# Kernel optimization log

Hardware: AMD Instinct MI355X
Metric: run time of the kernel (lower is better)

## Reference

```python
import jax, jax.numpy as jnp
import numpy as np

B, S, D_IN, D_OUT = 8, 2048, 1024, 1024


def setup_inputs() -> dict:
    key = jax.random.key(0)
    kx, kq, kk, kv = jax.random.split(key, 4)
    x = jax.random.normal(kx, (B, S, D_IN), dtype=jnp.float32)
    # torch nn.Linear weight is (d_out, d_in); we store the transpose (d_in, d_out)
    # and apply as x @ W, same math. Scale ~ kaiming-uniform-ish magnitude.
    scale = 1.0 / np.sqrt(D_IN)
    Wq = jax.random.normal(kq, (D_IN, D_OUT), dtype=jnp.float32) * scale
    Wk = jax.random.normal(kk, (D_IN, D_OUT), dtype=jnp.float32) * scale
    Wv = jax.random.normal(kv, (D_IN, D_OUT), dtype=jnp.float32) * scale
    return {"x": x, "Wq": Wq, "Wk": Wk, "Wv": Wv}


def reference(x, Wq, Wk, Wv):
    # x: (b, s, d_in) -> (b, s, d_out). Single-head causal attention, dropout=0.
    b, s, _ = x.shape
    q = jnp.einsum('bsd,de->bse', x, Wq)
    k = jnp.einsum('bsd,de->bse', x, Wk)
    v = jnp.einsum('bsd,de->bse', x, Wv)
    d_k = k.shape[-1]
    scores = jnp.einsum('bqe,bke->bqk', q, k) / jnp.sqrt(jnp.float32(d_k))
    # causal mask: position t attends to 0..t (strict upper triangle -> -inf)
    causal = jnp.tril(jnp.ones((s, s), dtype=bool))
    scores = jnp.where(causal[None, :, :], scores, -jnp.inf)
    weights = jax.nn.softmax(scores, axis=-1)
    return jnp.einsum('bqk,bke->bqe', weights, v)
```

## Files before the change

### kernel.cpp

```cpp
#include <hip/hip_runtime.h>


#define Bv 8
#define Sv 2048
#define Dv 1024
#define BK 32
#define NT 16

typedef _Float16 f16x8 __attribute__((ext_vector_type(8)));
typedef _Float16 f16x4 __attribute__((ext_vector_type(4)));
typedef float    f32x4 __attribute__((ext_vector_type(4)));

#define GLL(gp, lp)                                            \
  __builtin_amdgcn_global_load_lds(                            \
      (const __attribute__((address_space(1))) void*)(gp),     \
      (__attribute__((address_space(3))) void*)(lp), 16, 0, 0)

__device__ __forceinline__ void mma_step(const _Float16* As, const _Float16* Bs,
                                         int wm, int wn, int lane, f32x4 acc[4][4]) {
  int ll = lane & 15, quad = lane >> 4;
  f16x8 a[4], b[4];
#pragma unroll
  for (int mi = 0; mi < 4; ++mi)
    a[mi] = *(const f16x8*)(As + (wm * 64 + mi * 16 + ll) * BK + quad * 8);
#pragma unroll
  for (int ni = 0; ni < 4; ++ni)
    b[ni] = *(const f16x8*)(Bs + (wn * 64 + ni * 16 + ll) * BK + quad * 8);
#pragma unroll
  for (int mi = 0; mi < 4; ++mi)
#pragma unroll
    for (int ni = 0; ni < 4; ++ni)
      acc[mi][ni] = __builtin_amdgcn_mfma_f32_16x16x32_f16(a[mi], b[ni], acc[mi][ni], 0, 0, 0);
}

__device__ __forceinline__ void gemm_dbuf(const _Float16* __restrict__ A, int lda,
                                          const _Float16* __restrict__ B, int ldb,
                                          int ktiles, _Float16 (*S)[4096],
                                          f32x4 acc[4][4]) {
  const int tid  = threadIdx.x;
  const int lane = tid & 63, wave = tid >> 6;
  const int wm = wave >> 1, wn = wave & 1;
  const int srow = wave * 32 + (lane >> 2);
  const int scol = (lane & 3) * 8;
  const int loA0 = srow * lda + scol, loA1 = loA0 + 16 * lda;
  const int loB0 = srow * ldb + scol, loB1 = loB0 + 16 * ldb;
  _Float16* dA = &S[0][wave * 1024];
  _Float16* dB = &S[1][wave * 1024];
  const _Float16* gA = A;
  const _Float16* gB = B;

#define STAGE(bi)                              \
  do {                                         \
    GLL(gA + loA0, dA + (bi) * 8192);          \
    GLL(gA + loA1, dA + (bi) * 8192 + 512);    \
    GLL(gB + loB0, dB + (bi) * 8192);          \
    GLL(gB + loB1, dB + (bi) * 8192 + 512);    \
  } while (0)

  STAGE(0);
  for (int kt = 0; kt < ktiles; kt += 2) {
    __syncthreads();
    gA += BK; gB += BK;
    STAGE(1);
    mma_step(S[0], S[1], wm, wn, lane, acc);
    __syncthreads();
    gA += BK; gB += BK;
    if (kt + 2 < ktiles) STAGE(0);
    mma_step(S[2], S[3], wm, wn, lane, acc);
  }
#undef STAGE
}

#define ZERO_ACC(acc)                              \
  _Pragma("unroll") for (int i_ = 0; i_ < 4; ++i_) \
  _Pragma("unroll") for (int j_ = 0; j_ < 4; ++j_) \
      acc[i_][j_] = (f32x4){0.f, 0.f, 0.f, 0.f};

__global__ __launch_bounds__(256) void ca_cast(const float* __restrict__ x,
                                               _Float16* __restrict__ y) {
  int i = (blockIdx.x * 256 + threadIdx.x) * 8;
  f32x4 a = *(const f32x4*)(x + i);
  f32x4 b = *(const f32x4*)(x + i + 4);
  f16x8 h;
#pragma unroll
  for (int j = 0; j < 4; ++j) { h[j] = (_Float16)a[j]; h[4 + j] = (_Float16)b[j]; }
  *(f16x8*)(y + i) = h;
}

__global__ __launch_bounds__(256) void ca_transpose(const float* __restrict__ W0,
                                                    const float* __restrict__ W1,
                                                    const float* __restrict__ W2,
                                                    _Float16* __restrict__ T0,
                                                    _Float16* __restrict__ T1,
                                                    _Float16* __restrict__ T2) {
  const float* W = blockIdx.z == 0 ? W0 : blockIdx.z == 1 ? W1 : W2;
  _Float16* WT   = blockIdx.z == 0 ? T0 : blockIdx.z == 1 ? T1 : T2;
  __shared__ _Float16 t[32][33];
  int k0 = blockIdx.x * 32, n0 = blockIdx.y * 32;
  int r = threadIdx.x >> 5, c = threadIdx.x & 31;
#pragma unroll
  for (int i = 0; i < 4; ++i)
    t[r + i * 8][c] = (_Float16)W[(size_t)(k0 + r + i * 8) * Dv + n0 + c];
  __syncthreads();
#pragma unroll
  for (int i = 0; i < 4; ++i)
    WT[(size_t)(n0 + r + i * 8) * Dv + k0 + c] = t[c][r + i * 8];
}

__global__ __launch_bounds__(512, 2) void ca_qkv3(const _Float16* __restrict__ X,
                                                  const _Float16* __restrict__ WTq,
                                                  const _Float16* __restrict__ WTk,
                                                  const _Float16* __restrict__ WTv,
                                                  _Float16* __restrict__ Q,
                                                  _Float16* __restrict__ K,
                                                  _Float16* __restrict__ Vt) {
  __shared__ _Float16 L[8][8192];

  int id  = blockIdx.x;
  int swz = (id & 7) * 96 + (id >> 3);
  int my  = swz / 12, nt = swz - my * 12;
  int m0  = my * 256;
  int which = nt >> 2;
  int n0  = (nt & 3) * 256;
  const _Float16* WT = which == 0 ? WTq : which == 1 ? WTk : WTv;
  const _Float16* gA = X + (size_t)m0 * Dv;
  const _Float16* gB = WT + (size_t)n0 * Dv;

  const int tid  = threadIdx.x;
  const int lane = tid & 63, wave = tid >> 6;
  const int wm = wave >> 2, wn = wave & 3;
  const int ll = lane & 15, quad = lane >> 4;

  const int laneRow = wave * 8 + (lane >> 3);
  const int laneCol = (((lane & 7) ^ ((lane >> 3) & 7)) << 3);
  const int gOff0 = laneRow * Dv + laneCol;
  const int gOff1 = (64 + laneRow) * Dv + laneCol;
  _Float16* Ldst = &L[0][0] + wave * 512;

  const int sw0 = ((quad ^ (ll & 7)) << 3);
  _Float16* Lb = &L[0][0];
  const _Float16* pA0 = Lb + wm * 8192 + ll * 64 + sw0;
  const _Float16* pA1 = Lb + wm * 8192 + ll * 64 + (sw0 ^ 32);
  const _Float16* pB0 = Lb + 16384 + (wn >> 1) * 8192 + (wn & 1) * 4096 + ll * 64 + sw0;
  const _Float16* pB1 = Lb + 16384 + (wn >> 1) * 8192 + (wn & 1) * 4096 + ll * 64 + (sw0 ^ 32);

#define STG(slot, mat, ht, kpf)                                   \
  do {                                                            \
    const _Float16* g_ = (mat) + (size_t)((ht) * 128 * Dv + (kpf) * 64); \
    GLL(g_ + gOff0, Ldst + (slot) * 8192);                        \
    GLL(g_ + gOff1, Ldst + (slot) * 8192 + 4096);                 \
  } while (0)

#define RD_A(P, d, mh)                                            \
  _Pragma("unroll") for (int i_ = 0; i_ < 4; ++i_)                \
      a[i_] = *(const f16x8*)((P) + (d) * 32768 + ((mh) * 4 + i_) * 1024);
#define RD_B(P, d)                                                \
  _Pragma("unroll") for (int i_ = 0; i_ < 4; ++i_)                \
      b[i_] = *(const f16x8*)((P) + (d) * 32768 + i_ * 1024);
#define MMA(mh)                                                   \
  __builtin_amdgcn_s_setprio(1);                                  \
  _Pragma("unroll") for (int i_ = 0; i_ < 4; ++i_)                \
  _Pragma("unroll") for (int j_ = 0; j_ < 4; ++j_)                \
      acc[(mh) * 4 + i_][j_] = __builtin_amdgcn_mfma_f32_16x16x32_f16( \
          a[i_], b[j_], acc[(mh) * 4 + i_], 0, 0, 0)[0] == 0.f    \
          ? __builtin_amdgcn_mfma_f32_16x16x32_f16(a[i_], b[j_], acc[(mh) * 4 + i_][j_], 0, 0, 0) \
          : __builtin_amdgcn_mfma_f32_16x16x32_f16(a[i_], b[j_], acc[(mh) * 4 + i_][j_], 0, 0, 0); \
  __builtin_amdgcn_s_setprio(0);
#undef MMA
#define MMA(mh)                                                   \
  __builtin_amdgcn_s_setprio(1);                                  \
  _Pragma("unroll") for (int i_ = 0; i_ < 4; ++i_)                \
  _Pragma("unroll") for (int j_ = 0; j_ < 4; ++j_)                \
      acc[(mh) * 4 + i_][j_] = __builtin_amdgcn_mfma_f32_16x16x32_f16( \
          a[i_], b[j_], acc[(mh) * 4 + i_][j_], 0, 0, 0);         \
  __builtin_amdgcn_s_setprio(0);
#define BAR() __builtin_amdgcn_s_barrier()
#define WAITV_(n) asm volatile("s_waitcnt vmcnt(" #n ")" ::: "memory")
#define WAITV(n) WAITV_(n)
#define PH_OPEN()                                                 \
  BAR();                                                          \
  asm volatile("s_waitcnt lgkmcnt(0)" ::: "memory");              \
  __builtin_amdgcn_sched_barrier(0)

#define TILEG(kk, d, G)                                           \
  do {                                                            \
    f16x8 a[4], b[4];                                             \
    RD_A(pA0, d, 0); RD_B(pB0, d);                                \
    if ((kk) + 1 < NT) STG(4 * (1 - (d)) + 0, gA, 0, (kk) + 1);   \
    PH_OPEN(); MMA(0); BAR();                                     \
    RD_A(pA0, d, 1);                                              \
    if ((kk) + 1 < NT) STG(4 * (1 - (d)) + 1, gA, 1, (kk) + 1);   \
    PH_OPEN(); MMA(1); BAR();                                     \
    RD_A(pA1, d, 0); RD_B(pB1, d);                                \
    if ((kk) + 1 < NT) STG(4 * (1 - (d)) + 3, gB, 1, (kk) + 1);   \
    PH_OPEN(); MMA(0); BAR();                                     \
    __builtin_amdgcn_sched_barrier(0);                            \
    RD_A(pA1, d, 1);                                              \
    if ((kk) + 2 < NT) STG(4 * (d) + 2, gB, 0, (kk) + 2);         \
    PH_OPEN(); MMA(1);                                            \
    WAITV(G); BAR();                                              \
    __builtin_amdgcn_sched_barrier(0);                            \
  } while (0)

  f32x4 acc[8][4];
#pragma unroll
  for (int i = 0; i < 8; ++i)
#pragma unroll
    for (int j = 0; j < 4; ++j) acc[i][j] = (f32x4){0.f, 0.f, 0.f, 0.f};

  STG(2, gB, 0, 0);
  STG(0, gA, 0, 0);
  STG(1, gA, 1, 0);
  STG(3, gB, 1, 0);
  STG(6, gB, 0, 1);
  WAITV(2); BAR();
  __builtin_amdgcn_sched_barrier(0);

#pragma unroll 1
  for (int kk = 0; kk < NT - 2; kk += 2) {
    TILEG(kk, 0, 2);
    TILEG(kk + 1, 1, 2);
  }
  TILEG(14, 0, 0);
  TILEG(15, 1, 2);

#undef TILEG
#undef PH_OPEN
#undef MMA
#undef RD_A
#undef RD_B
#undef STG

  if (which < 2) {
    _Float16* Out = which == 0 ? Q : K;
#pragma unroll
    for (int mi = 0; mi < 8; ++mi)
#pragma unroll
      for (int ni = 0; ni < 4; ++ni) {
        int gc = n0 + wn * 64 + ni * 16 + ll;
#pragma unroll
        for (int r = 0; r < 4; ++r) {
          int gr = m0 + wm * 128 + mi * 16 + quad * 4 + r;
          Out[(size_t)gr * Dv + gc] = (_Float16)acc[mi][ni][r];
        }
      }
  } else {
#pragma unroll
    for (int mi = 0; mi < 8; ++mi)
#pragma unroll
      for (int ni = 0; ni < 4; ++ni) {
        int gc = n0 + wn * 64 + ni * 16 + ll;
        int gr = m0 + wm * 128 + mi * 16 + quad * 4;
        f16x4 v;
#pragma unroll
        for (int r = 0; r < 4; ++r) v[r] = (_Float16)acc[mi][ni][r];
        *(f16x4*)(Vt + (size_t)gc * (Bv * Sv) + gr) = v;
      }
  }
}

__global__ __launch_bounds__(256) void ca_score(const _Float16* __restrict__ Q,
                                                const _Float16* __restrict__ Km,
                                                _Float16* __restrict__ U) {
  int kt = blockIdx.x, qt = blockIdx.y, b = blockIdx.z;
  if (kt > qt) return;
  __shared__ _Float16 S[4][4096];
  f32x4 acc[4][4];
  ZERO_ACC(acc);
  const _Float16* Qb = Q + ((size_t)b * Sv + qt * 128) * Dv;
  const _Float16* Kb = Km + ((size_t)b * Sv + kt * 128) * Dv;
  gemm_dbuf(Qb, Dv, Kb, Dv, Dv / BK, S, acc);
  int lane = threadIdx.x & 63, wave = threadIdx.x >> 6;
  int wm = wave >> 1, wn = wave & 1, ll = lane & 15, quad = lane >> 4;
#pragma unroll
  for (int mi = 0; mi < 4; ++mi)
#pragma unroll
    for (int ni = 0; ni < 4; ++ni) {
      int kc = kt * 128 + wn * 64 + ni * 16 + ll;
#pragma unroll
      for (int r = 0; r < 4; ++r) {
        int qr = qt * 128 + wm * 64 + mi * 16 + quad * 4 + r;
        float s = acc[mi][ni][r] * 0.03125f;
        float u = (kc > qr) ? 0.f : __expf(fminf(fmaxf(s, -15.f), 10.f));
        U[((size_t)b * Sv + qr) * Sv + kc] = (_Float16)u;
      }
    }
}

__global__ __launch_bounds__(256) void ca_rowsum(const _Float16* __restrict__ U,
                                                 float* __restrict__ invl) {
  int rg = blockIdx.x;
  int b = rg >> 11, q = rg & (Sv - 1);
  int lim = ((q >> 7) + 1) << 7;
  const _Float16* row = U + ((size_t)b * Sv + q) * Sv;
  float s = 0.f;
  for (int k = threadIdx.x * 8; k < lim; k += 2048) {
    f16x8 v = *(const f16x8*)(row + k);
#pragma unroll
    for (int j = 0; j < 8; ++j) s += (float)v[j];
  }
#pragma unroll
  for (int o = 32; o >= 1; o >>= 1) s += __shfl_down(s, o);
  __shared__ float wsum[4];
  if ((threadIdx.x & 63) == 0) wsum[threadIdx.x >> 6] = s;
  __syncthreads();
  if (threadIdx.x == 0) invl[rg] = 1.f / (wsum[0] + wsum[1] + wsum[2] + wsum[3]);
}

__global__ __launch_bounds__(256) void ca_pv(const _Float16* __restrict__ U,
                                             const _Float16* __restrict__ Vt,
                                             const float* __restrict__ invl,
                                             float* __restrict__ Out) {
  int nt = blockIdx.x, qt = blockIdx.y, b = blockIdx.z;
  __shared__ _Float16 S[4][4096];
  f32x4 acc[4][4];
  ZERO_ACC(acc);
  const _Float16* Ab = U + ((size_t)b * Sv + qt * 128) * Sv;
  const _Float16* Bb = Vt + (size_t)(nt * 128) * (Bv * Sv) + (size_t)b * Sv;
  gemm_dbuf(Ab, Sv, Bb, Bv * Sv, (qt + 1) * 4, S, acc);
  int lane = threadIdx.x & 63, wave = threadIdx.x >> 6;
  int wm = wave >> 1, wn = wave & 1, ll = lane & 15, quad = lane >> 4;
#pragma unroll
  for (int mi = 0; mi < 4; ++mi)
#pragma unroll
    for (int ni = 0; ni < 4; ++ni) {
      int oc = nt * 128 + wn * 64 + ni * 16 + ll;
#pragma unroll
      for (int r = 0; r < 4; ++r) {
        int qr = qt * 128 + wm * 64 + mi * 16 + quad * 4 + r;
        Out[((size_t)b * Sv + qr) * Dv + oc] = acc[mi][ni][r] * invl[b * Sv + qr];
      }
    }
}

extern "C" void kernel_launch(void* const* d_in, const int* in_sizes, int n_in,
                              void* d_out, int out_size, void* d_ws, size_t ws_size,
                              hipStream_t stream) {
  const float* x  = (const float*)d_in[0];
  const float* Wq = (const float*)d_in[1];
  const float* Wk = (const float*)d_in[2];
  const float* Wv = (const float*)d_in[3];
  float* out = (float*)d_out;

  char* ws = (char*)d_ws;
  size_t off = 0;
  const size_t M = (size_t)Bv * Sv;
  _Float16* xh  = (_Float16*)(ws + off); off += M * Dv * 2;
  _Float16* WTq = (_Float16*)(ws + off); off += (size_t)Dv * Dv * 2;
  _Float16* WTk = (_Float16*)(ws + off); off += (size_t)Dv * Dv * 2;
  _Float16* WTv = (_Float16*)(ws + off); off += (size_t)Dv * Dv * 2;
  _Float16* Q   = (_Float16*)(ws + off); off += M * Dv * 2;
  _Float16* Km  = (_Float16*)(ws + off); off += M * Dv * 2;
  _Float16* Vt  = (_Float16*)(ws + off); off += M * Dv * 2;
  _Float16* U   = (_Float16*)(ws + off); off += (size_t)Bv * Sv * Sv * 2;
  float*    invl = (float*)(ws + off);   off += M * 4;

  ca_cast<<<(M * Dv) / (8 * 256), 256, 0, stream>>>(x, xh);
  ca_transpose<<<dim3(32, 32, 3), 256, 0, stream>>>(Wq, Wk, Wv, WTq, WTk, WTv);

  ca_qkv3<<<dim3(768), 512, 0, stream>>>(xh, WTq, WTk, WTv, Q, Km, Vt);

  ca_score<<<dim3(Sv / 128, Sv / 128, Bv), 256, 0, stream>>>(Q, Km, U);
  ca_rowsum<<<M, 256, 0, stream>>>(U, invl);
  ca_pv<<<dim3(Dv / 128, Sv / 128, Bv), 256, 0, stream>>>(U, Vt, invl, out);
}
```

Measured before the change: 405.2 us.

## Reuse the tuned 256x256 GEMM mainloop for the score and PV kernels

The pipelined, swizzled 256x256 mainloop from the QKV projection kernel becomes a generic gemm_fine function with configurable leading dimensions and K-tile count. The score and PV kernels now use it with 512-thread blocks, replacing the simpler 128x128 double-buffered GEMM. The goal is more data reuse per block and a better MFMA/LDS pipeline for the two attention GEMMs. The cost is coarser causal tiles, which waste more work on the diagonal, and far fewer blocks (288 score and 256 PV) with unequal work per block, which can leave CUs idle.

```diff
diff --git a/kernel.cpp b/kernel.cpp
--- a/kernel.cpp
+++ b/kernel.cpp
@@ -4,8 +4,7 @@
 #define Bv 8
 #define Sv 2048
 #define Dv 1024
-#define BK 32
-#define NT 16
+#define NTQ 16
 
 typedef _Float16 f16x8 __attribute__((ext_vector_type(8)));
 typedef _Float16 f16x4 __attribute__((ext_vector_type(4)));
@@ -15,66 +14,6 @@
   __builtin_amdgcn_global_load_lds(                            \
       (const __attribute__((address_space(1))) void*)(gp),     \
       (__attribute__((address_space(3))) void*)(lp), 16, 0, 0)
-
-__device__ __forceinline__ void mma_step(const _Float16* As, const _Float16* Bs,
-                                         int wm, int wn, int lane, f32x4 acc[4][4]) {
-  int ll = lane & 15, quad = lane >> 4;
-  f16x8 a[4], b[4];
-#pragma unroll
-  for (int mi = 0; mi < 4; ++mi)
-    a[mi] = *(const f16x8*)(As + (wm * 64 + mi * 16 + ll) * BK + quad * 8);
-#pragma unroll
-  for (int ni = 0; ni < 4; ++ni)
-    b[ni] = *(const f16x8*)(Bs + (wn * 64 + ni * 16 + ll) * BK + quad * 8);
-#pragma unroll
-  for (int mi = 0; mi < 4; ++mi)
-#pragma unroll
-    for (int ni = 0; ni < 4; ++ni)
-      acc[mi][ni] = __builtin_amdgcn_mfma_f32_16x16x32_f16(a[mi], b[ni], acc[mi][ni], 0, 0, 0);
-}
-
-__device__ __forceinline__ void gemm_dbuf(const _Float16* __restrict__ A, int lda,
-                                          const _Float16* __restrict__ B, int ldb,
-                                          int ktiles, _Float16 (*S)[4096],
-                                          f32x4 acc[4][4]) {
-  const int tid  = threadIdx.x;
-  const int lane = tid & 63, wave = tid >> 6;
-  const int wm = wave >> 1, wn = wave & 1;
-  const int srow = wave * 32 + (lane >> 2);
-  const int scol = (lane & 3) * 8;
-  const int loA0 = srow * lda + scol, loA1 = loA0 + 16 * lda;
-  const int loB0 = srow * ldb + scol, loB1 = loB0 + 16 * ldb;
-  _Float16* dA = &S[0][wave * 1024];
-  _Float16* dB = &S[1][wave * 1024];
-  const _Float16* gA = A;
-  const _Float16* gB = B;
-
-#define STAGE(bi)                              \
-  do {                                         \
-    GLL(gA + loA0, dA + (bi) * 8192);          \
-    GLL(gA + loA1, dA + (bi) * 8192 + 512);    \
-    GLL(gB + loB0, dB + (bi) * 8192);          \
-    GLL(gB + loB1, dB + (bi) * 8192 + 512);    \
-  } while (0)
-
-  STAGE(0);
-  for (int kt = 0; kt < ktiles; kt += 2) {
-    __syncthreads();
-    gA += BK; gB += BK;
-    STAGE(1);
-    mma_step(S[0], S[1], wm, wn, lane, acc);
-    __syncthreads();
-    gA += BK; gB += BK;
-    if (kt + 2 < ktiles) STAGE(0);
-    mma_step(S[2], S[3], wm, wn, lane, acc);
-  }
-#undef STAGE
-}
-
-#define ZERO_ACC(acc)                              \
-  _Pragma("unroll") for (int i_ = 0; i_ < 4; ++i_) \
-  _Pragma("unroll") for (int j_ = 0; j_ < 4; ++j_) \
-      acc[i_][j_] = (f32x4){0.f, 0.f, 0.f, 0.f};
 
 __global__ __launch_bounds__(256) void ca_cast(const float* __restrict__ x,
                                                _Float16* __restrict__ y) {
@@ -107,25 +46,10 @@
     WT[(size_t)(n0 + r + i * 8) * Dv + k0 + c] = t[c][r + i * 8];
 }
 
-__global__ __launch_bounds__(512, 2) void ca_qkv3(const _Float16* __restrict__ X,
-                                                  const _Float16* __restrict__ WTq,
-                                                  const _Float16* __restrict__ WTk,
-                                                  const _Float16* __restrict__ WTv,
-                                                  _Float16* __restrict__ Q,
-                                                  _Float16* __restrict__ K,
-                                                  _Float16* __restrict__ Vt) {
-  __shared__ _Float16 L[8][8192];
-
-  int id  = blockIdx.x;
-  int swz = (id & 7) * 96 + (id >> 3);
-  int my  = swz / 12, nt = swz - my * 12;
-  int m0  = my * 256;
-  int which = nt >> 2;
-  int n0  = (nt & 3) * 256;
-  const _Float16* WT = which == 0 ? WTq : which == 1 ? WTk : WTv;
-  const _Float16* gA = X + (size_t)m0 * Dv;
-  const _Float16* gB = WT + (size_t)n0 * Dv;
-
+__device__ __forceinline__ void gemm_fine(const _Float16* __restrict__ gA, int ldA,
+                                          const _Float16* __restrict__ gB, long ldB,
+                                          int NTt, _Float16 (*L)[8192],
+                                          f32x4 acc[8][4]) {
   const int tid  = threadIdx.x;
   const int lane = tid & 63, wave = tid >> 6;
   const int wm = wave >> 2, wn = wave & 3;
@@ -133,8 +57,10 @@
 
   const int laneRow = wave * 8 + (lane >> 3);
   const int laneCol = (((lane & 7) ^ ((lane >> 3) & 7)) << 3);
-  const int gOff0 = laneRow * Dv + laneCol;
-  const int gOff1 = (64 + laneRow) * Dv + laneCol;
+  const long aOff0 = (long)laneRow * ldA + laneCol;
+  const long aOff1 = (long)(64 + laneRow) * ldA + laneCol;
+  const long bOff0 = (long)laneRow * ldB + laneCol;
+  const long bOff1 = (long)(64 + laneRow) * ldB + laneCol;
   _Float16* Ldst = &L[0][0] + wave * 512;
 
   const int sw0 = ((quad ^ (ll & 7)) << 3);
@@ -144,29 +70,24 @@
   const _Float16* pB0 = Lb + 16384 + (wn >> 1) * 8192 + (wn & 1) * 4096 + ll * 64 + sw0;
   const _Float16* pB1 = Lb + 16384 + (wn >> 1) * 8192 + (wn & 1) * 4096 + ll * 64 + (sw0 ^ 32);
 
-#define STG(slot, mat, ht, kpf)                                   \
+#define STGA(slot, ht, kpf)                                       \
   do {                                                            \
-    const _Float16* g_ = (mat) + (size_t)((ht) * 128 * Dv + (kpf) * 64); \
-    GLL(g_ + gOff0, Ldst + (slot) * 8192);                        \
-    GLL(g_ + gOff1, Ldst + (slot) * 8192 + 4096);                 \
+    const _Float16* g_ = gA + (long)(ht) * 128 * ldA + (long)(kpf) * 64; \
+    GLL(g_ + aOff0, Ldst + (slot) * 8192);                        \
+    GLL(g_ + aOff1, Ldst + (slot) * 8192 + 4096);                 \
   } while (0)
-
+#define STGB(slot, ht, kpf)                                       \
+  do {                                                            \
+    const _Float16* g_ = gB + (long)(ht) * 128 * ldB + (long)(kpf) * 64; \
+    GLL(g_ + bOff0, Ldst + (slot) * 8192);                        \
+    GLL(g_ + bOff1, Ldst + (slot) * 8192 + 4096);                 \
+  } while (0)
 #define RD_A(P, d, mh)                                            \
   _Pragma("unroll") for (int i_ = 0; i_ < 4; ++i_)                \
       a[i_] = *(const f16x8*)((P) + (d) * 32768 + ((mh) * 4 + i_) * 1024);
 #define RD_B(P, d)                                                \
   _Pragma("unroll") for (int i_ = 0; i_ < 4; ++i_)                \
       b[i_] = *(const f16x8*)((P) + (d) * 32768 + i_ * 1024);
-#define MMA(mh)                                                   \
-  __builtin_amdgcn_s_setprio(1);                                  \
-  _Pragma("unroll") for (int i_ = 0; i_ < 4; ++i_)                \
-  _Pragma("unroll") for (int j_ = 0; j_ < 4; ++j_)                \
-      acc[(mh) * 4 + i_][j_] = __builtin_amdgcn_mfma_f32_16x16x32_f16( \
-          a[i_], b[j_], acc[(mh) * 4 + i_], 0, 0, 0)[0] == 0.f    \
-          ? __builtin_amdgcn_mfma_f32_16x16x32_f16(a[i_], b[j_], acc[(mh) * 4 + i_][j_], 0, 0, 0) \
-          : __builtin_amdgcn_mfma_f32_16x16x32_f16(a[i_], b[j_], acc[(mh) * 4 + i_][j_], 0, 0, 0); \
-  __builtin_amdgcn_s_setprio(0);
-#undef MMA
 #define MMA(mh)                                                   \
   __builtin_amdgcn_s_setprio(1);                                  \
   _Pragma("unroll") for (int i_ = 0; i_ < 4; ++i_)                \
@@ -186,51 +107,76 @@
   do {                                                            \
     f16x8 a[4], b[4];                                             \
     RD_A(pA0, d, 0); RD_B(pB0, d);                                \
-    if ((kk) + 1 < NT) STG(4 * (1 - (d)) + 0, gA, 0, (kk) + 1);   \
+    if ((kk) + 1 < NTt) STGA(4 * (1 - (d)) + 0, 0, (kk) + 1);     \
     PH_OPEN(); MMA(0); BAR();                                     \
     RD_A(pA0, d, 1);                                              \
-    if ((kk) + 1 < NT) STG(4 * (1 - (d)) + 1, gA, 1, (kk) + 1);   \
+    if ((kk) + 1 < NTt) STGA(4 * (1 - (d)) + 1, 1, (kk) + 1);     \
     PH_OPEN(); MMA(1); BAR();                                     \
     RD_A(pA1, d, 0); RD_B(pB1, d);                                \
-    if ((kk) + 1 < NT) STG(4 * (1 - (d)) + 3, gB, 1, (kk) + 1);   \
+    if ((kk) + 1 < NTt) STGB(4 * (1 - (d)) + 3, 1, (kk) + 1);     \
     PH_OPEN(); MMA(0); BAR();                                     \
     __builtin_amdgcn_sched_barrier(0);                            \
     RD_A(pA1, d, 1);                                              \
-    if ((kk) + 2 < NT) STG(4 * (d) + 2, gB, 0, (kk) + 2);         \
+    if ((kk) + 2 < NTt) STGB(4 * (d) + 2, 0, (kk) + 2);           \
     PH_OPEN(); MMA(1);                                            \
     WAITV(G); BAR();                                              \
     __builtin_amdgcn_sched_barrier(0);                            \
   } while (0)
 
-  f32x4 acc[8][4];
-#pragma unroll
-  for (int i = 0; i < 8; ++i)
-#pragma unroll
-    for (int j = 0; j < 4; ++j) acc[i][j] = (f32x4){0.f, 0.f, 0.f, 0.f};
-
-  STG(2, gB, 0, 0);
-  STG(0, gA, 0, 0);
-  STG(1, gA, 1, 0);
-  STG(3, gB, 1, 0);
-  STG(6, gB, 0, 1);
+  STGB(2, 0, 0);
+  STGA(0, 0, 0);
+  STGA(1, 1, 0);
+  STGB(3, 1, 0);
+  STGB(6, 0, 1);
   WAITV(2); BAR();
   __builtin_amdgcn_sched_barrier(0);
 
 #pragma unroll 1
-  for (int kk = 0; kk < NT - 2; kk += 2) {
+  for (int kk = 0; kk < NTt - 2; kk += 2) {
     TILEG(kk, 0, 2);
     TILEG(kk + 1, 1, 2);
   }
-  TILEG(14, 0, 0);
-  TILEG(15, 1, 2);
+  TILEG(NTt - 2, 0, 0);
+  TILEG(NTt - 1, 1, 2);
 
 #undef TILEG
 #undef PH_OPEN
 #undef MMA
 #undef RD_A
 #undef RD_B
-#undef STG
-
+#undef STGB
+#undef STGA
+}
+
+#define ZERO8x4(acc)                               \
+  _Pragma("unroll") for (int i_ = 0; i_ < 8; ++i_) \
+  _Pragma("unroll") for (int j_ = 0; j_ < 4; ++j_) \
+      acc[i_][j_] = (f32x4){0.f, 0.f, 0.f, 0.f};
+
+__global__ __launch_bounds__(512, 2) void ca_qkv3(const _Float16* __restrict__ X,
+                                                  const _Float16* __restrict__ WTq,
+                                                  const _Float16* __restrict__ WTk,
+                                                  const _Float16* __restrict__ WTv,
+                                                  _Float16* __restrict__ Q,
+                                                  _Float16* __restrict__ K,
+                                                  _Float16* __restrict__ Vt) {
+  __shared__ _Float16 L[8][8192];
+
+  int id  = blockIdx.x;
+  int swz = (id & 7) * 96 + (id >> 3);
+  int my  = swz / 12, nt = swz - my * 12;
+  int m0  = my * 256;
+  int which = nt >> 2;
+  int n0  = (nt & 3) * 256;
+  const _Float16* WT = which == 0 ? WTq : which == 1 ? WTk : WTv;
+
+  f32x4 acc[8][4];
+  ZERO8x4(acc);
+  gemm_fine(X + (size_t)m0 * Dv, Dv, WT + (size_t)n0 * Dv, Dv, NTQ, L, acc);
+
+  const int lane = threadIdx.x & 63, wave = threadIdx.x >> 6;
+  const int wm = wave >> 2, wn = wave & 3;
+  const int ll = lane & 15, quad = lane >> 4;
   if (which < 2) {
     _Float16* Out = which == 0 ? Q : K;
 #pragma unroll
@@ -259,27 +205,29 @@
   }
 }
 
-__global__ __launch_bounds__(256) void ca_score(const _Float16* __restrict__ Q,
-                                                const _Float16* __restrict__ Km,
-                                                _Float16* __restrict__ U) {
+__global__ __launch_bounds__(512, 2) void ca_score2(const _Float16* __restrict__ Q,
+                                                    const _Float16* __restrict__ Km,
+                                                    _Float16* __restrict__ U) {
   int kt = blockIdx.x, qt = blockIdx.y, b = blockIdx.z;
   if (kt > qt) return;
-  __shared__ _Float16 S[4][4096];
-  f32x4 acc[4][4];
-  ZERO_ACC(acc);
-  const _Float16* Qb = Q + ((size_t)b * Sv + qt * 128) * Dv;
-  const _Float16* Kb = Km + ((size_t)b * Sv + kt * 128) * Dv;
-  gemm_dbuf(Qb, Dv, Kb, Dv, Dv / BK, S, acc);
-  int lane = threadIdx.x & 63, wave = threadIdx.x >> 6;
-  int wm = wave >> 1, wn = wave & 1, ll = lane & 15, quad = lane >> 4;
-#pragma unroll
-  for (int mi = 0; mi < 4; ++mi)
+  __shared__ _Float16 L[8][8192];
+  f32x4 acc[8][4];
+  ZERO8x4(acc);
+  const _Float16* Qb = Q + ((size_t)b * Sv + qt * 256) * Dv;
+  const _Float16* Kb = Km + ((size_t)b * Sv + kt * 256) * Dv;
+  gemm_fine(Qb, Dv, Kb, Dv, NTQ, L, acc);
+
+  const int lane = threadIdx.x & 63, wave = threadIdx.x >> 6;
+  const int wm = wave >> 2, wn = wave & 3;
+  const int ll = lane & 15, quad = lane >> 4;
+#pragma unroll
+  for (int mi = 0; mi < 8; ++mi)
 #pragma unroll
     for (int ni = 0; ni < 4; ++ni) {
-      int kc = kt * 128 + wn * 64 + ni * 16 + ll;
+      int kc = kt * 256 + wn * 64 + ni * 16 + ll;
 #pragma unroll
       for (int r = 0; r < 4; ++r) {
-        int qr = qt * 128 + wm * 64 + mi * 16 + quad * 4 + r;
+        int qr = qt * 256 + wm * 128 + mi * 16 + quad * 4 + r;
         float s = acc[mi][ni][r] * 0.03125f;
         float u = (kc > qr) ? 0.f : __expf(fminf(fmaxf(s, -15.f), 10.f));
         U[((size_t)b * Sv + qr) * Sv + kc] = (_Float16)u;
@@ -307,27 +255,29 @@
   if (threadIdx.x == 0) invl[rg] = 1.f / (wsum[0] + wsum[1] + wsum[2] + wsum[3]);
 }
 
-__global__ __launch_bounds__(256) void ca_pv(const _Float16* __restrict__ U,
-                                             const _Float16* __restrict__ Vt,
-                                             const float* __restrict__ invl,
-                                             float* __restrict__ Out) {
+__global__ __launch_bounds__(512, 2) void ca_pv2(const _Float16* __restrict__ U,
+                                                 const _Float16* __restrict__ Vt,
+                                                 const float* __restrict__ invl,
+                                                 float* __restrict__ Out) {
   int nt = blockIdx.x, qt = blockIdx.y, b = blockIdx.z;
-  __shared__ _Float16 S[4][4096];
-  f32x4 acc[4][4];
-  ZERO_ACC(acc);
-  const _Float16* Ab = U + ((size_t)b * Sv + qt * 128) * Sv;
-  const _Float16* Bb = Vt + (size_t)(nt * 128) * (Bv * Sv) + (size_t)b * Sv;
-  gemm_dbuf(Ab, Sv, Bb, Bv * Sv, (qt + 1) * 4, S, acc);
-  int lane = threadIdx.x & 63, wave = threadIdx.x >> 6;
-  int wm = wave >> 1, wn = wave & 1, ll = lane & 15, quad = lane >> 4;
-#pragma unroll
-  for (int mi = 0; mi < 4; ++mi)
+  __shared__ _Float16 L[8][8192];
+  f32x4 acc[8][4];
+  ZERO8x4(acc);
+  const _Float16* Ab = U + ((size_t)b * Sv + qt * 256) * Sv;
+  const _Float16* Bb = Vt + (size_t)(nt * 256) * (Bv * Sv) + (size_t)b * Sv;
+  gemm_fine(Ab, Sv, Bb, (long)Bv * Sv, (qt + 1) * 4, L, acc);
+
+  const int lane = threadIdx.x & 63, wave = threadIdx.x >> 6;
+  const int wm = wave >> 2, wn = wave & 3;
+  const int ll = lane & 15, quad = lane >> 4;
+#pragma unroll
+  for (int mi = 0; mi < 8; ++mi)
 #pragma unroll
     for (int ni = 0; ni < 4; ++ni) {
-      int oc = nt * 128 + wn * 64 + ni * 16 + ll;
+      int oc = nt * 256 + wn * 64 + ni * 16 + ll;
 #pragma unroll
       for (int r = 0; r < 4; ++r) {
-        int qr = qt * 128 + wm * 64 + mi * 16 + quad * 4 + r;
+        int qr = qt * 256 + wm * 128 + mi * 16 + quad * 4 + r;
         Out[((size_t)b * Sv + qr) * Dv + oc] = acc[mi][ni][r] * invl[b * Sv + qr];
       }
     }
@@ -360,7 +310,7 @@
 
   ca_qkv3<<<dim3(768), 512, 0, stream>>>(xh, WTq, WTk, WTv, Q, Km, Vt);
 
-  ca_score<<<dim3(Sv / 128, Sv / 128, Bv), 256, 0, stream>>>(Q, Km, U);
+  ca_score2<<<dim3(8, 8, Bv), 512, 0, stream>>>(Q, Km, U);
   ca_rowsum<<<M, 256, 0, stream>>>(U, invl);
-  ca_pv<<<dim3(Dv / 128, Sv / 128, Bv), 256, 0, stream>>>(U, Vt, invl, out);
-}
+  ca_pv2<<<dim3(4, 8, Bv), 512, 0, stream>>>(U, Vt, invl, out);
+}
```

Result: faster. 359.6 us (-11.2%).
